# Optimization experiments

Hardware: AMD Instinct MI355X
Metric: run time of the kernel (lower is better)

## Reference

```python
import jax, jax.numpy as jnp
from jax import lax
import numpy as np

GC_LAMBDA = 0.75
N = 8388608  # chain length (number of graph nodes between source and sink)


def setup_inputs() -> dict:
    key = jax.random.key(0)
    inputs = jax.random.uniform(key, (N,), dtype=jnp.float32)  # probabilities in [0,1)
    return {"inputs": inputs}


def reference(inputs):
    # Min s-t cut of the chain graph == Viterbi DP over binary labels x_i:
    #   E(x) = sum_i [x_i==1 ? (1-p_i) : p_i] + lam * sum_{i>0} [x_i != x_{i-1}]
    # Label 1 <=> node on source side (reachable set) in the min cut.
    lam = jnp.float32(GC_LAMBDA)
    cost0 = inputs          # x_i = 0: cut source->i edge, capacity p_i
    cost1 = 1.0 - inputs    # x_i = 1: cut i->sink edge, capacity 1 - p_i

    def fwd(carry, costs):
        a0, a1 = carry       # best energy ending in state 0 / 1 (renormalized)
        c0, c1 = costs
        from1 = a1 + lam < a0   # best predecessor of current state 0 is state 1
        from0 = a0 + lam < a1   # best predecessor of current state 1 is state 0
        n0 = c0 + jnp.minimum(a0, a1 + lam)
        n1 = c1 + jnp.minimum(a1, a0 + lam)
        m = jnp.minimum(n0, n1)  # keep carries small for fp32 accuracy over long chains
        return (n0 - m, n1 - m), (from1, from0)

    (a0, a1), (from1, from0) = lax.scan(
        fwd, (cost0[0], cost1[0]), (cost0[1:], cost1[1:])
    )
    last = a1 < a0  # label of the final node (True -> 1)

    def bwd(state, chs):
        f1, f0 = chs
        prev = jnp.where(state, ~f0, f1)  # backtrack the argmin pointers
        return prev, prev

    _, states = lax.scan(bwd, last, (from1, from0), reverse=True)
    labels = jnp.concatenate([states, last[None]])  # [N] bool
    return labels.astype(jnp.int32)
```

## Files before the change

### kernel.cpp

```cpp
#include <hip/hip_runtime.h>
#include <stdint.h>


#define LAM 0.75f
constexpr int N_TOTAL = 8388608;
constexpr int SEG = 64;
constexpr int NSEG = N_TOTAL / SEG;
constexpr int NBLK = NSEG / 256;

__device__ __forceinline__ float dstep(float d, float p) {
    float e0 = fminf(fmaxf(d, 0.0f), LAM);
    float e1 = fminf(fmaxf(-d, 0.0f), LAM);
    return (p + e0) - ((1.0f - p) + e1);
}

__device__ float seg0_end(const float* __restrict__ p) {
    float p0 = p[0];
    float a0 = p0, a1 = 1.0f - p0;
    float t0 = fminf(a0, a1 + LAM);
    float t1 = fminf(a1, a0 + LAM);
    float p1 = p[1];
    float d = (p1 + t0) - ((1.0f - p1) + t1);
    for (int i = 2; i < 64; ++i) d = dstep(d, p[i]);
    return d;
}

union SegU { float4 q[16]; float f[64]; };

__global__ __launch_bounds__(256) void k_ab(const float* __restrict__ p,
        uint64_t* __restrict__ ev, uint64_t* __restrict__ sg) {
    __shared__ float s_dh[256];
    __shared__ uint8_t s_ok[256];
    const int t = threadIdx.x;
    const int s = blockIdx.x * 256 + t;

    SegU u;
    const float4* g4 = (const float4*)(p + (size_t)s * SEG);
    #pragma unroll
    for (int i = 0; i < 16; ++i) u.q[i] = g4[i];

    float dh = 2.0f, dl = -2.0f;
    #pragma unroll
    for (int i = 0; i < 64; ++i) {
        float pi = u.f[i];
        dh = dstep(dh, pi);
        dl = dstep(dl, pi);
    }
    s_dh[t] = dh;
    s_ok[t] = (dh == dl) ? 1 : 0;
    __syncthreads();

    float d = 0.0f;
    uint64_t e = 0, gw = 0;
    if (s == 0) {
        float p0 = u.f[0];
        float a0 = p0, a1 = 1.0f - p0;
        bool f1 = (a1 + LAM) < a0;
        bool f0 = (a0 + LAM) < a1;
        e |= (uint64_t)(f1 || f0); gw |= (uint64_t)f1;
        float t0 = fminf(a0, a1 + LAM);
        float t1 = fminf(a1, a0 + LAM);
        float p1 = u.f[1];
        d = (p1 + t0) - ((1.0f - p1) + t1);
        e |= (uint64_t)(d > LAM || d < -LAM) << 1;
        gw |= (uint64_t)(d > LAM) << 1;
        #pragma unroll
        for (int i = 2; i < 64; ++i) {
            d = dstep(d, u.f[i]);
            e  |= (uint64_t)(d > LAM || d < -LAM) << i;
            gw |= (uint64_t)(d > LAM) << i;
        }
    } else {
        int back = t - 1;
        while (back >= 0 && !s_ok[back]) --back;
        int startSeg;
        if (back >= 0) {
            d = s_dh[back];
            startSeg = blockIdx.x * 256 + back;
        } else {
            int v = blockIdx.x * 256 - 1;
            for (;;) {
                if (v == 0) { d = seg0_end(p); startSeg = 0; break; }
                const float4* gv = (const float4*)(p + (size_t)v * SEG);
                float h = 2.0f, l = -2.0f;
                for (int i = 0; i < 16; ++i) {
                    float4 q = gv[i];
                    h = dstep(h, q.x); l = dstep(l, q.x);
                    h = dstep(h, q.y); l = dstep(l, q.y);
                    h = dstep(h, q.z); l = dstep(l, q.z);
                    h = dstep(h, q.w); l = dstep(l, q.w);
                }
                if (h == l) { d = h; startSeg = v; break; }
                --v;
            }
        }
        for (int v = startSeg + 1; v < s; ++v) {
            const float* sv = p + (size_t)v * SEG;
            for (int i = 0; i < 64; ++i) d = dstep(d, sv[i]);
        }
        #pragma unroll
        for (int i = 0; i < 64; ++i) {
            d = dstep(d, u.f[i]);
            e  |= (uint64_t)(d > LAM || d < -LAM) << i;
            gw |= (uint64_t)(d > LAM) << i;
        }
    }
    if (s == NSEG - 1) {
        const uint64_t top = 1ull << 63;
        e |= top;
        gw = (d > 0.0f) ? (gw | top) : (gw & ~top);
    }
    ev[s] = e;
    sg[s] = gw;
}

__global__ __launch_bounds__(256) void k_fill(const uint64_t* __restrict__ ev,
        const uint64_t* __restrict__ sg, int* __restrict__ out) {
    __shared__ uint64_t lev[256];
    __shared__ uint64_t lsg[256];
    __shared__ int lC[256];
    const int t = threadIdx.x;
    const int b = blockIdx.x;
    const int w = b * 256 + t;

    uint64_t e = ev[w], g = sg[w];
    lev[t] = e; lsg[t] = g;
    __syncthreads();

    int cur = 0; bool found = false;
    for (int v = t + 1; v < 256; ++v) {
        uint64_t evv = lev[v];
        if (evv) { cur = (int)((lsg[v] >> __builtin_ctzll(evv)) & 1ull); found = true; break; }
    }
    if (!found && b + 1 < NBLK) {
        int v = (b + 1) * 256;
        while (v < NSEG) {
            uint64_t evv = ev[v];
            if (evv) { cur = (int)((sg[v] >> __builtin_ctzll(evv)) & 1ull); break; }
            ++v;
        }
    }
    lC[t] = cur;
    __syncthreads();

    int4* o4 = (int4*)out + (size_t)b * 4096;
    #pragma unroll
    for (int i = 0; i < 16; ++i) {
        int c = i * 256 + t;
        int wl = c >> 4;
        int bb = (c & 15) * 4;
        uint64_t we = lev[wl], wg = lsg[wl];
        int wc = lC[wl];
        int4 r;
        {
            uint64_t m = we >> (bb + 0);
            r.x = m ? (int)((wg >> (bb + 0 + __builtin_ctzll(m))) & 1ull) : wc;
            m = we >> (bb + 1);
            r.y = m ? (int)((wg >> (bb + 1 + __builtin_ctzll(m))) & 1ull) : wc;
            m = we >> (bb + 2);
            r.z = m ? (int)((wg >> (bb + 2 + __builtin_ctzll(m))) & 1ull) : wc;
            m = we >> (bb + 3);
            r.w = m ? (int)((wg >> (bb + 3 + __builtin_ctzll(m))) & 1ull) : wc;
        }
        o4[c] = r;
    }
}

extern "C" void kernel_launch(void* const* d_in, const int* in_sizes, int n_in,
                              void* d_out, int out_size, void* d_ws, size_t ws_size,
                              hipStream_t stream) {
    (void)in_sizes; (void)n_in; (void)out_size; (void)ws_size;
    const float* p = (const float*)d_in[0];
    int* out = (int*)d_out;
    char* ws = (char*)d_ws;
    uint64_t* ev = (uint64_t*)ws;
    uint64_t* sg = (uint64_t*)(ws + (size_t)NSEG * 8);

    k_ab<<<dim3(NBLK), dim3(256), 0, stream>>>(p, ev, sg);
    k_fill<<<dim3(NBLK), dim3(256), 0, stream>>>(ev, sg, out);
}
```

Measured before the change: 89.41 us.

## Halve segment length to 32 and interleave event/sign masks in one array

Shrinks each thread's segment from 64 to 32 elements, which doubles the thread count in the forward kernel and shortens each thread's serial dependency chain. Event and sign bitmasks are now stored as interleaved 32-bit pairs, so the fill kernel reads two adjacent segments as a single uint4 and rebuilds 64-bit words. Launch bounds now request 4 blocks per CU. Shorter segments can make the backward search for a converged segment longer, and more threads may fall back to replaying earlier segments serially.

```diff
diff --git a/kernel.cpp b/kernel.cpp
--- a/kernel.cpp
+++ b/kernel.cpp
@@ -4,9 +4,11 @@
 
 #define LAM 0.75f
 constexpr int N_TOTAL = 8388608;
-constexpr int SEG = 64;
+constexpr int SEG = 32;
 constexpr int NSEG = N_TOTAL / SEG;
-constexpr int NBLK = NSEG / 256;
+constexpr int NBLK_AB = NSEG / 256;
+constexpr int NWORD = N_TOTAL / 64;
+constexpr int NBLK_FILL = NWORD / 256;
 
 __device__ __forceinline__ float dstep(float d, float p) {
     float e0 = fminf(fmaxf(d, 0.0f), LAM);
@@ -21,14 +23,14 @@
     float t1 = fminf(a1, a0 + LAM);
     float p1 = p[1];
     float d = (p1 + t0) - ((1.0f - p1) + t1);
-    for (int i = 2; i < 64; ++i) d = dstep(d, p[i]);
+    for (int i = 2; i < SEG; ++i) d = dstep(d, p[i]);
     return d;
 }
 
-union SegU { float4 q[16]; float f[64]; };
+union SegU { float4 q[8]; float f[32]; };
 
-__global__ __launch_bounds__(256) void k_ab(const float* __restrict__ p,
-        uint64_t* __restrict__ ev, uint64_t* __restrict__ sg) {
+__global__ __launch_bounds__(256, 4) void k_ab(const float* __restrict__ p,
+        uint2* __restrict__ evsg) {
     __shared__ float s_dh[256];
     __shared__ uint8_t s_ok[256];
     const int t = threadIdx.x;
@@ -37,11 +39,11 @@
     SegU u;
     const float4* g4 = (const float4*)(p + (size_t)s * SEG);
     #pragma unroll
-    for (int i = 0; i < 16; ++i) u.q[i] = g4[i];
+    for (int i = 0; i < 8; ++i) u.q[i] = g4[i];
 
     float dh = 2.0f, dl = -2.0f;
     #pragma unroll
-    for (int i = 0; i < 64; ++i) {
+    for (int i = 0; i < SEG; ++i) {
         float pi = u.f[i];
         dh = dstep(dh, pi);
         dl = dstep(dl, pi);
@@ -51,24 +53,24 @@
     __syncthreads();
 
     float d = 0.0f;
-    uint64_t e = 0, gw = 0;
+    uint32_t em = 0, gm = 0;
     if (s == 0) {
         float p0 = u.f[0];
         float a0 = p0, a1 = 1.0f - p0;
         bool f1 = (a1 + LAM) < a0;
         bool f0 = (a0 + LAM) < a1;
-        e |= (uint64_t)(f1 || f0); gw |= (uint64_t)f1;
+        em |= (uint32_t)(f1 || f0); gm |= (uint32_t)f1;
         float t0 = fminf(a0, a1 + LAM);
         float t1 = fminf(a1, a0 + LAM);
         float p1 = u.f[1];
         d = (p1 + t0) - ((1.0f - p1) + t1);
-        e |= (uint64_t)(d > LAM || d < -LAM) << 1;
-        gw |= (uint64_t)(d > LAM) << 1;
+        em |= (uint32_t)(fabsf(d) > LAM) << 1;
+        gm |= (uint32_t)(d > LAM) << 1;
         #pragma unroll
-        for (int i = 2; i < 64; ++i) {
+        for (int i = 2; i < SEG; ++i) {
             d = dstep(d, u.f[i]);
-            e  |= (uint64_t)(d > LAM || d < -LAM) << i;
-            gw |= (uint64_t)(d > LAM) << i;
+            em |= (uint32_t)(fabsf(d) > LAM) << i;
+            gm |= (uint32_t)(d > LAM) << i;
         }
     } else {
         int back = t - 1;
@@ -83,7 +85,7 @@
                 if (v == 0) { d = seg0_end(p); startSeg = 0; break; }
                 const float4* gv = (const float4*)(p + (size_t)v * SEG);
                 float h = 2.0f, l = -2.0f;
-                for (int i = 0; i < 16; ++i) {
+                for (int i = 0; i < 8; ++i) {
                     float4 q = gv[i];
                     h = dstep(h, q.x); l = dstep(l, q.x);
                     h = dstep(h, q.y); l = dstep(l, q.y);
@@ -96,26 +98,24 @@
         }
         for (int v = startSeg + 1; v < s; ++v) {
             const float* sv = p + (size_t)v * SEG;
-            for (int i = 0; i < 64; ++i) d = dstep(d, sv[i]);
+            for (int i = 0; i < SEG; ++i) d = dstep(d, sv[i]);
         }
         #pragma unroll
-        for (int i = 0; i < 64; ++i) {
+        for (int i = 0; i < SEG; ++i) {
             d = dstep(d, u.f[i]);
-            e  |= (uint64_t)(d > LAM || d < -LAM) << i;
-            gw |= (uint64_t)(d > LAM) << i;
+            em |= (uint32_t)(fabsf(d) > LAM) << i;
+            gm |= (uint32_t)(d > LAM) << i;
         }
     }
     if (s == NSEG - 1) {
-        const uint64_t top = 1ull << 63;
-        e |= top;
-        gw = (d > 0.0f) ? (gw | top) : (gw & ~top);
+        em |= 0x80000000u;
+        gm = (d > 0.0f) ? (gm | 0x80000000u) : (gm & 0x7FFFFFFFu);
     }
-    ev[s] = e;
-    sg[s] = gw;
+    evsg[s] = make_uint2(em, gm);
 }
 
-__global__ __launch_bounds__(256) void k_fill(const uint64_t* __restrict__ ev,
-        const uint64_t* __restrict__ sg, int* __restrict__ out) {
+__global__ __launch_bounds__(256, 4) void k_fill(const uint4* __restrict__ evsg2,
+        int* __restrict__ out) {
     __shared__ uint64_t lev[256];
     __shared__ uint64_t lsg[256];
     __shared__ int lC[256];
@@ -123,7 +123,9 @@
     const int b = blockIdx.x;
     const int w = b * 256 + t;
 
-    uint64_t e = ev[w], g = sg[w];
+    uint4 wv = evsg2[w];
+    uint64_t e = ((uint64_t)wv.z << 32) | wv.x;
+    uint64_t g = ((uint64_t)wv.w << 32) | wv.y;
     lev[t] = e; lsg[t] = g;
     __syncthreads();
 
@@ -132,11 +134,16 @@
         uint64_t evv = lev[v];
         if (evv) { cur = (int)((lsg[v] >> __builtin_ctzll(evv)) & 1ull); found = true; break; }
     }
-    if (!found && b + 1 < NBLK) {
+    if (!found && b + 1 < NBLK_FILL) {
         int v = (b + 1) * 256;
-        while (v < NSEG) {
-            uint64_t evv = ev[v];
-            if (evv) { cur = (int)((sg[v] >> __builtin_ctzll(evv)) & 1ull); break; }
+        while (v < NWORD) {
+            uint4 sv = evsg2[v];
+            uint64_t evv = ((uint64_t)sv.z << 32) | sv.x;
+            if (evv) {
+                uint64_t sgv = ((uint64_t)sv.w << 32) | sv.y;
+                cur = (int)((sgv >> __builtin_ctzll(evv)) & 1ull);
+                break;
+            }
             ++v;
         }
     }
@@ -152,16 +159,14 @@
         uint64_t we = lev[wl], wg = lsg[wl];
         int wc = lC[wl];
         int4 r;
-        {
-            uint64_t m = we >> (bb + 0);
-            r.x = m ? (int)((wg >> (bb + 0 + __builtin_ctzll(m))) & 1ull) : wc;
-            m = we >> (bb + 1);
-            r.y = m ? (int)((wg >> (bb + 1 + __builtin_ctzll(m))) & 1ull) : wc;
-            m = we >> (bb + 2);
-            r.z = m ? (int)((wg >> (bb + 2 + __builtin_ctzll(m))) & 1ull) : wc;
-            m = we >> (bb + 3);
-            r.w = m ? (int)((wg >> (bb + 3 + __builtin_ctzll(m))) & 1ull) : wc;
-        }
+        uint64_t m = we >> (bb + 0);
+        r.x = m ? (int)((wg >> (bb + 0 + __builtin_ctzll(m))) & 1ull) : wc;
+        m = we >> (bb + 1);
+        r.y = m ? (int)((wg >> (bb + 1 + __builtin_ctzll(m))) & 1ull) : wc;
+        m = we >> (bb + 2);
+        r.z = m ? (int)((wg >> (bb + 2 + __builtin_ctzll(m))) & 1ull) : wc;
+        m = we >> (bb + 3);
+        r.w = m ? (int)((wg >> (bb + 3 + __builtin_ctzll(m))) & 1ull) : wc;
         o4[c] = r;
     }
 }
@@ -172,10 +177,8 @@
     (void)in_sizes; (void)n_in; (void)out_size; (void)ws_size;
     const float* p = (const float*)d_in[0];
     int* out = (int*)d_out;
-    char* ws = (char*)d_ws;
-    uint64_t* ev = (uint64_t*)ws;
-    uint64_t* sg = (uint64_t*)(ws + (size_t)NSEG * 8);
+    uint2* evsg = (uint2*)d_ws;
 
-    k_ab<<<dim3(NBLK), dim3(256), 0, stream>>>(p, ev, sg);
-    k_fill<<<dim3(NBLK), dim3(256), 0, stream>>>(ev, sg, out);
+    k_ab<<<dim3(NBLK_AB), dim3(256), 0, stream>>>(p, evsg);
+    k_fill<<<dim3(NBLK_FILL), dim3(256), 0, stream>>>((const uint4*)evsg, out);
 }
```

Measured after the change: 87.15 us. -2.5%, faster.
